# Kernel tuning notes

Hardware: AMD Instinct MI355X
Metric: run time of the kernel (lower is better)

The kernel has to match this reference:

```python
import jax, jax.numpy as jnp
import numpy as np

B, T, D, H, L = 64, 4096, 128, 128, 2


def setup_inputs() -> dict:
    key = jax.random.key(0)
    ks = jax.random.split(key, 9)
    s = 1.0 / np.sqrt(H)
    return {
        "x": jax.random.normal(ks[0], (B, T, D), dtype=jnp.float32),
        "W_ih0": jax.random.normal(ks[1], (3 * H, D), dtype=jnp.float32) * s,
        "W_hh0": jax.random.normal(ks[2], (3 * H, H), dtype=jnp.float32) * s,
        "b_ih0": jax.random.normal(ks[3], (3 * H,), dtype=jnp.float32) * s,
        "b_hh0": jax.random.normal(ks[4], (3 * H,), dtype=jnp.float32) * s,
        "W_ih1": jax.random.normal(ks[5], (3 * H, H), dtype=jnp.float32) * s,
        "W_hh1": jax.random.normal(ks[6], (3 * H, H), dtype=jnp.float32) * s,
        "b_ih1": jax.random.normal(ks[7], (3 * H,), dtype=jnp.float32) * s,
        "b_hh1": jax.random.normal(ks[8], (3 * H,), dtype=jnp.float32) * s,
    }


def _gru_cell(h, xt, W_ih, W_hh, b_ih, b_hh):
    # torch.nn.GRUCell math; gates packed as [r, z, n] along 3H.
    gi = xt @ W_ih.T + b_ih            # [B, 3H]
    gh = h @ W_hh.T + b_hh             # [B, 3H]
    i_r, i_z, i_n = jnp.split(gi, 3, axis=-1)
    h_r, h_z, h_n = jnp.split(gh, 3, axis=-1)
    r = jax.nn.sigmoid(i_r + h_r)
    z = jax.nn.sigmoid(i_z + h_z)
    n = jnp.tanh(i_n + r * h_n)
    return (1.0 - z) * n + z * h


def reference(x, W_ih0, W_hh0, b_ih0, b_hh0, W_ih1, W_hh1, b_ih1, b_hh1):
    h0 = jnp.zeros((L, x.shape[0], H), dtype=x.dtype)
    params = ((W_ih0, W_hh0, b_ih0, b_hh0), (W_ih1, W_hh1, b_ih1, b_hh1))

    def step(h, xt):
        # h: [L, B, H]; xt: [B, D]
        inp = xt
        new_h = []
        for l in range(L):
            hl = _gru_cell(h[l], inp, *params[l])
            new_h.append(hl)
            inp = hl
        return jnp.stack(new_h, axis=0), None

    xs = jnp.swapaxes(x, 0, 1)  # [T, B, D]
    h_final, _ = jax.lax.scan(step, h0, xs)
    return h_final  # [L, B, H]
```

## Files before the change

### kernel.cpp

```cpp
#include <hip/hip_runtime.h>
#include <cmath>


#define Bsz  64
#define Tlen 4096
#define Din  128
#define Hd   128

typedef __attribute__((ext_vector_type(8))) short short8;
typedef __attribute__((ext_vector_type(4))) short short4v;
typedef __attribute__((ext_vector_type(4))) float float4v;

#define MFMA16(a, b, c) __builtin_amdgcn_mfma_f32_16x16x32_bf16((a), (b), (c), 0, 0, 0)

static __device__ __forceinline__ short f2bf(float f) {
  unsigned u = __builtin_bit_cast(unsigned, f);
  u = (u + 0x7FFFu + ((u >> 16) & 1u)) >> 16;
  return (short)u;
}

static __device__ __forceinline__ float sigm(float x) {
  return __builtin_amdgcn_rcpf(1.0f + __expf(-x));
}

static __device__ __forceinline__ float tanh_f(float x) {
  x = fmaxf(x, -30.0f);
  float e = __expf(-2.0f * x);
  return (1.0f - e) * __builtin_amdgcn_rcpf(1.0f + e);
}

static __device__ __forceinline__ short8 loadw8(const float* __restrict__ p) {
  short8 r;
  #pragma unroll
  for (int j = 0; j < 8; ++j) r[j] = f2bf(p[j]);
  return r;
}

#define STRIDE 520

__global__ __launch_bounds__(512, 2) void gru_scan(
    const float* __restrict__ x,
    const float* __restrict__ Wih0, const float* __restrict__ Whh0,
    const float* __restrict__ bih0, const float* __restrict__ bhh0,
    const float* __restrict__ Wih1, const float* __restrict__ Whh1,
    const float* __restrict__ bih1, const float* __restrict__ bhh1,
    float* __restrict__ out) {
  __shared__ alignas(16) short Abuf[16 * STRIDE];

  const int tid   = threadIdx.x;
  const int wave  = tid >> 6;
  const int lane  = tid & 63;
  const int lc    = lane & 15;
  const int quad  = lane >> 4;
  const int q8    = quad * 8;
  const int bbase = blockIdx.x * 16;

  const int nr = wave * 16 + lc;
  const int nz = 128 + wave * 16 + lc;
  const int nn = 256 + wave * 16 + lc;

  short8 fr0[8], fz0[8], fin0[4], fhn0[4];
  short8 fr1[8], fz1[8], fin1[4], fhn1[4];
  #pragma unroll
  for (int s = 0; s < 4; ++s) {
    const int k = 32 * s + q8;
    fr0[s]     = loadw8(Wih0 + nr * Din + k);
    fz0[s]     = loadw8(Wih0 + nz * Din + k);
    fin0[s]    = loadw8(Wih0 + nn * Din + k);
    fr0[s + 4] = loadw8(Whh0 + nr * Hd + k);
    fz0[s + 4] = loadw8(Whh0 + nz * Hd + k);
    fhn0[s]    = loadw8(Whh0 + nn * Hd + k);
    fr1[s]     = loadw8(Wih1 + nr * Hd + k);
    fz1[s]     = loadw8(Wih1 + nz * Hd + k);
    fin1[s]    = loadw8(Wih1 + nn * Hd + k);
    fr1[s + 4] = loadw8(Whh1 + nr * Hd + k);
    fz1[s + 4] = loadw8(Whh1 + nz * Hd + k);
    fhn1[s]    = loadw8(Whh1 + nn * Hd + k);
  }

  const float br0 = bih0[nr] + bhh0[nr];
  const float bz0 = bih0[nz] + bhh0[nz];
  const float bi0 = bih0[nn];
  const float bh0 = bhh0[nn];
  const float br1 = bih1[nr] + bhh1[nr];
  const float bz1 = bih1[nz] + bhh1[nz];
  const float bi1 = bih1[nn];
  const float bh1 = bhh1[nn];

  for (int i = tid; i < 16 * STRIDE; i += 512) Abuf[i] = 0;
  __syncthreads();

  const int xrow = tid >> 5;
  const int xd   = (tid & 31) * 4;
  const float* xbase = x + (size_t)(bbase + xrow) * Tlen * Din + xd;
  {
    const float4v xv = *(const float4v*)xbase;
    short4v s4;
    #pragma unroll
    for (int j = 0; j < 4; ++j) s4[j] = f2bf(xv[j]);
    *(short4v*)&Abuf[xrow * STRIDE + xd] = s4;
  }
  __syncthreads();

  float h0p[4] = {0.f, 0.f, 0.f, 0.f};
  float h1p[4] = {0.f, 0.f, 0.f, 0.f};
  const int aoff = lc * STRIDE + q8;

  #pragma unroll 2
  for (int t = 0; t < Tlen; ++t) {
    const int tn = (t + 1 < Tlen) ? t + 1 : t;
    const float4v xv = *(const float4v*)(xbase + (size_t)tn * Din);

    float4v ar = {0.f, 0.f, 0.f, 0.f}, az = {0.f, 0.f, 0.f, 0.f};
    float4v ain = {0.f, 0.f, 0.f, 0.f}, ahn = {0.f, 0.f, 0.f, 0.f};
    #pragma unroll
    for (int s = 0; s < 4; ++s) {
      const short8 a = *(const short8*)&Abuf[aoff + 32 * s];
      ar  = MFMA16(a, fr0[s], ar);
      az  = MFMA16(a, fz0[s], az);
      ain = MFMA16(a, fin0[s], ain);
    }
    #pragma unroll
    for (int s = 0; s < 4; ++s) {
      const short8 a = *(const short8*)&Abuf[aoff + 128 + 32 * s];
      ar  = MFMA16(a, fr0[s + 4], ar);
      az  = MFMA16(a, fz0[s + 4], az);
      ahn = MFMA16(a, fhn0[s], ahn);
    }
    __syncthreads();

    float h0n[4];
    #pragma unroll
    for (int i = 0; i < 4; ++i) {
      const float r  = sigm(ar[i] + br0);
      const float z  = sigm(az[i] + bz0);
      const float nn_ = tanh_f(ain[i] + bi0 + r * (ahn[i] + bh0));
      h0n[i] = z * (h0p[i] - nn_) + nn_;
      h0p[i] = h0n[i];
    }
    #pragma unroll
    for (int i = 0; i < 4; ++i)
      Abuf[(quad * 4 + i) * STRIDE + 128 + wave * 16 + lc] = f2bf(h0n[i]);
    {
      short4v s4;
      #pragma unroll
      for (int j = 0; j < 4; ++j) s4[j] = f2bf(xv[j]);
      *(short4v*)&Abuf[xrow * STRIDE + xd] = s4;
    }
    __syncthreads();

    const int rb = 256 + 128 * (t & 1);
    const int wb = 256 + 128 * ((t & 1) ^ 1);
    float4v cr = {0.f, 0.f, 0.f, 0.f}, cz = {0.f, 0.f, 0.f, 0.f};
    float4v cin = {0.f, 0.f, 0.f, 0.f}, chn = {0.f, 0.f, 0.f, 0.f};
    #pragma unroll
    for (int s = 0; s < 4; ++s) {
      const short8 a = *(const short8*)&Abuf[aoff + 128 + 32 * s];
      cr  = MFMA16(a, fr1[s], cr);
      cz  = MFMA16(a, fz1[s], cz);
      cin = MFMA16(a, fin1[s], cin);
    }
    #pragma unroll
    for (int s = 0; s < 4; ++s) {
      const short8 a = *(const short8*)&Abuf[aoff + rb + 32 * s];
      cr  = MFMA16(a, fr1[s + 4], cr);
      cz  = MFMA16(a, fz1[s + 4], cz);
      chn = MFMA16(a, fhn1[s], chn);
    }
    #pragma unroll
    for (int i = 0; i < 4; ++i) {
      const float r  = sigm(cr[i] + br1);
      const float z  = sigm(cz[i] + bz1);
      const float nn_ = tanh_f(cin[i] + bi1 + r * (chn[i] + bh1));
      const float h  = z * (h1p[i] - nn_) + nn_;
      h1p[i] = h;
      Abuf[(quad * 4 + i) * STRIDE + wb + wave * 16 + lc] = f2bf(h);
    }
  }

  #pragma unroll
  for (int i = 0; i < 4; ++i) {
    const int b = bbase + quad * 4 + i;
    const int h = wave * 16 + lc;
    out[b * Hd + h]            = h0p[i];
    out[Bsz * Hd + b * Hd + h] = h1p[i];
  }
}

extern "C" void kernel_launch(void* const* d_in, const int* in_sizes, int n_in,
                              void* d_out, int out_size, void* d_ws, size_t ws_size,
                              hipStream_t stream) {
  (void)in_sizes; (void)n_in; (void)out_size; (void)d_ws; (void)ws_size;
  gru_scan<<<4, 512, 0, stream>>>(
      (const float*)d_in[0],
      (const float*)d_in[1], (const float*)d_in[2],
      (const float*)d_in[3], (const float*)d_in[4],
      (const float*)d_in[5], (const float*)d_in[6],
      (const float*)d_in[7], (const float*)d_in[8],
      (float*)d_out);
}
```

Baseline: 8.490 ms.

## Software-pipeline GRU layers across phases with swizzled LDS and exp2 gates

Restructures the per-timestep loop into two phases so that layer-1 gate math for step t-1 is interleaved with layer-0 MFMAs for step t, and layer-0 gate math overlaps layer-1 MFMAs. This hides transcendental latency behind matrix work while keeping two barriers per step. It also replaces the padded row-major LDS layout with a fragment-ordered layout so each lane reads one contiguous short8. Gate activations fold log2(e) scaling into exp2 and packed bf16 conversions. The added prologue and epilogue make the ping-pong indexing more complex and easier to get wrong.

Measured after the change: 13.14 ms. 1.55x slower.

```diff
diff --git a/kernel.cpp b/kernel.cpp
--- a/kernel.cpp
+++ b/kernel.cpp
@@ -1,5 +1,4 @@
 #include <hip/hip_runtime.h>
-#include <cmath>
 
 
 #define Bsz  64
@@ -10,25 +9,33 @@
 typedef __attribute__((ext_vector_type(8))) short short8;
 typedef __attribute__((ext_vector_type(4))) short short4v;
 typedef __attribute__((ext_vector_type(4))) float float4v;
+typedef __attribute__((ext_vector_type(2))) unsigned int uintx2;
 
 #define MFMA16(a, b, c) __builtin_amdgcn_mfma_f32_16x16x32_bf16((a), (b), (c), 0, 0, 0)
 
+static __device__ __forceinline__ float fast_exp2(float x) {
+#if __has_builtin(__builtin_amdgcn_exp2f)
+  return __builtin_amdgcn_exp2f(x);
+#else
+  return exp2f(x);
+#endif
+}
+static __device__ __forceinline__ float fast_rcp(float x) {
+  return __builtin_amdgcn_rcpf(x);
+}
 static __device__ __forceinline__ short f2bf(float f) {
   unsigned u = __builtin_bit_cast(unsigned, f);
   u = (u + 0x7FFFu + ((u >> 16) & 1u)) >> 16;
   return (short)u;
 }
-
-static __device__ __forceinline__ float sigm(float x) {
-  return __builtin_amdgcn_rcpf(1.0f + __expf(-x));
-}
-
-static __device__ __forceinline__ float tanh_f(float x) {
-  x = fmaxf(x, -30.0f);
-  float e = __expf(-2.0f * x);
-  return (1.0f - e) * __builtin_amdgcn_rcpf(1.0f + e);
-}
-
+static __device__ __forceinline__ unsigned pk2bf(float a, float b) {
+#if __has_builtin(__builtin_amdgcn_cvt_pk_bf16_f32)
+  auto v = __builtin_amdgcn_cvt_pk_bf16_f32(a, b);
+  return __builtin_bit_cast(unsigned, v);
+#else
+  return (unsigned)(unsigned short)f2bf(a) | ((unsigned)(unsigned short)f2bf(b) << 16);
+#endif
+}
 static __device__ __forceinline__ short8 loadw8(const float* __restrict__ p) {
   short8 r;
   #pragma unroll
@@ -36,7 +43,6 @@
   return r;
 }
 
-#define STRIDE 520
 
 __global__ __launch_bounds__(512, 2) void gru_scan(
     const float* __restrict__ x,
@@ -45,7 +51,7 @@
     const float* __restrict__ Wih1, const float* __restrict__ Whh1,
     const float* __restrict__ bih1, const float* __restrict__ bhh1,
     float* __restrict__ out) {
-  __shared__ alignas(16) short Abuf[16 * STRIDE];
+  __shared__ alignas(16) short Abuf[10240];
 
   const int tid   = threadIdx.x;
   const int wave  = tid >> 6;
@@ -53,6 +59,7 @@
   const int lc    = lane & 15;
   const int quad  = lane >> 4;
   const int q8    = quad * 8;
+  const int lane8 = lane * 8;
   const int bbase = blockIdx.x * 16;
 
   const int nr = wave * 16 + lc;
@@ -78,112 +85,178 @@
     fhn1[s]    = loadw8(Whh1 + nn * Hd + k);
   }
 
-  const float br0 = bih0[nr] + bhh0[nr];
-  const float bz0 = bih0[nz] + bhh0[nz];
-  const float bi0 = bih0[nn];
-  const float bh0 = bhh0[nn];
-  const float br1 = bih1[nr] + bhh1[nr];
-  const float bz1 = bih1[nz] + bhh1[nz];
-  const float bi1 = bih1[nn];
-  const float bh1 = bhh1[nn];
-
-  for (int i = tid; i < 16 * STRIDE; i += 512) Abuf[i] = 0;
-  __syncthreads();
-
-  const int xrow = tid >> 5;
-  const int xd   = (tid & 31) * 4;
-  const float* xbase = x + (size_t)(bbase + xrow) * Tlen * Din + xd;
+  const float nL  = -1.44269504088896f;
+  const float n2L = -2.88539008177793f;
+  const float kr0 = nL * (bih0[nr] + bhh0[nr]);
+  const float kz0 = nL * (bih0[nz] + bhh0[nz]);
+  const float ki0 = n2L * bih0[nn];
+  const float kh0 = n2L * bhh0[nn];
+  const float kr1 = nL * (bih1[nr] + bhh1[nr]);
+  const float kz1 = nL * (bih1[nz] + bhh1[nz]);
+  const float ki1 = n2L * bih1[nn];
+  const float kh1 = n2L * bhh1[nn];
+
+  const int col    = wave * 16 + lc;
+  const int hwbase = ((col >> 5) << 9) + (((col >> 3) & 3) << 7) + (col & 7);
+
+  const int xrow = (tid >> 1) & 15;
+  const int xcol = ((tid >> 7) << 5) + (((tid >> 5) & 3) << 3) + ((tid & 1) << 2);
+  const float* xg = x + (size_t)(bbase + xrow) * (Tlen * Din) + xcol;
+  const int xw = 4 * tid;
+
   {
-    const float4v xv = *(const float4v*)xbase;
-    short4v s4;
-    #pragma unroll
-    for (int j = 0; j < 4; ++j) s4[j] = f2bf(xv[j]);
-    *(short4v*)&Abuf[xrow * STRIDE + xd] = s4;
-  }
-  __syncthreads();
-
+    int* zb = (int*)Abuf;
+    #pragma unroll
+    for (int i = 0; i < 8; ++i) zb[1024 + tid + 512 * i] = 0;
+    const float4v v0 = *(const float4v*)(xg);
+    const unsigned p0 = pk2bf(v0[0], v0[1]);
+    const unsigned p1 = pk2bf(v0[2], v0[3]);
+    uintx2 pp = {p0, p1};
+    *(short4v*)&Abuf[xw] = __builtin_bit_cast(short4v, pp);
+  }
+  __syncthreads();
+
+  const float4v Z4 = {0.f, 0.f, 0.f, 0.f};
+  float4v Ar = Z4, Az = Z4, Ain = Z4, Ahn = Z4;
+  float4v Cr = Z4, Cz = Z4, Cin = Z4, Chn = Z4;
   float h0p[4] = {0.f, 0.f, 0.f, 0.f};
   float h1p[4] = {0.f, 0.f, 0.f, 0.f};
-  const int aoff = lc * STRIDE + q8;
-
-  #pragma unroll 2
-  for (int t = 0; t < Tlen; ++t) {
-    const int tn = (t + 1 < Tlen) ? t + 1 : t;
-    const float4v xv = *(const float4v*)(xbase + (size_t)tn * Din);
-
-    float4v ar = {0.f, 0.f, 0.f, 0.f}, az = {0.f, 0.f, 0.f, 0.f};
-    float4v ain = {0.f, 0.f, 0.f, 0.f}, ahn = {0.f, 0.f, 0.f, 0.f};
+  float4v xv;
+  int t;
+
+#define GATE(acc_r, acc_z, acc_in, acc_hn, KR, KZ, KI, KH, hp, dst, S)        \
+  {                                                                           \
+    const float er = fast_exp2(fmaf((acc_r)[S], nL, (KR)));                   \
+    const float rr = fast_rcp(1.0f + er);                                     \
+    const float ez = fast_exp2(fmaf((acc_z)[S], nL, (KZ)));                   \
+    const float zz = fast_rcp(1.0f + ez);                                     \
+    float vv = fmaf(rr, fmaf((acc_hn)[S], n2L, (KH)),                         \
+                    fmaf((acc_in)[S], n2L, (KI)));                            \
+    vv = fminf(vv, 126.0f);                                                   \
+    const float e2 = fast_exp2(vv);                                           \
+    const float nn_ = (1.0f - e2) * fast_rcp(1.0f + e2);                      \
+    (dst)[S] = fmaf(zz, (hp)[S] - nn_, nn_);                                  \
+    (hp)[S] = (dst)[S];                                                       \
+  }
+
+#define PH_A(P, DOV1)                                                         \
+  {                                                                           \
+    const int tn = (t + 1 < Tlen) ? (t + 1) : (Tlen - 1);                     \
+    xv = *(const float4v*)(xg + (size_t)tn * Din);                            \
+    Ar = Z4; Az = Z4; Ain = Z4; Ahn = Z4;                                     \
+    float h1n[4];                                                             \
+    _Pragma("unroll")                                                         \
+    for (int s = 0; s < 4; ++s) {                                             \
+      const short8 a = *(const short8*)&Abuf[s * 512 + lane8];                \
+      Ar  = MFMA16(a, fr0[s], Ar);                                            \
+      Az  = MFMA16(a, fz0[s], Az);                                            \
+      Ain = MFMA16(a, fin0[s], Ain);                                          \
+      if (DOV1) GATE(Cr, Cz, Cin, Chn, kr1, kz1, ki1, kh1, h1p, h1n, s)       \
+    }                                                                         \
+    _Pragma("unroll")                                                         \
+    for (int s = 0; s < 4; ++s) {                                             \
+      const short8 a =                                                        \
+          *(const short8*)&Abuf[2048 + ((P) ^ 1) * 2048 + s * 512 + lane8];   \
+      Ar  = MFMA16(a, fr0[4 + s], Ar);                                        \
+      Az  = MFMA16(a, fz0[4 + s], Az);                                        \
+      Ahn = MFMA16(a, fhn0[s], Ahn);                                          \
+      if ((DOV1) && (s & 1)) {                                                \
+        const unsigned pk = pk2bf(h1n[s - 1], h1n[s]);                        \
+        Abuf[6144 + (P) * 2048 + hwbase + (quad * 4 + s - 1) * 8] =           \
+            (short)pk;                                                        \
+        Abuf[6144 + (P) * 2048 + hwbase + (quad * 4 + s) * 8] =               \
+            (short)(pk >> 16);                                                \
+      }                                                                       \
+    }                                                                         \
+  }                                                                           \
+  __syncthreads();
+
+#define PH_B(P, DOC)                                                          \
+  {                                                                           \
+    float h0n[4];                                                             \
+    if (DOC) { Cr = Z4; Cz = Z4; Cin = Z4; Chn = Z4; }                        \
+    _Pragma("unroll")                                                         \
+    for (int s = 0; s < 4; ++s) {                                             \
+      if (DOC) {                                                              \
+        const short8 a =                                                      \
+            *(const short8*)&Abuf[2048 + ((P) ^ 1) * 2048 + s * 512 + lane8]; \
+        Cr  = MFMA16(a, fr1[s], Cr);                                          \
+        Cz  = MFMA16(a, fz1[s], Cz);                                          \
+        Cin = MFMA16(a, fin1[s], Cin);                                        \
+      }                                                                       \
+      GATE(Ar, Az, Ain, Ahn, kr0, kz0, ki0, kh0, h0p, h0n, s)                 \
+    }                                                                         \
+    _Pragma("unroll")                                                         \
+    for (int s = 0; s < 4; ++s) {                                             \
+      if (DOC) {                                                              \
+        const short8 a =                                                      \
+            *(const short8*)&Abuf[6144 + (P) * 2048 + s * 512 + lane8];       \
+        Cr  = MFMA16(a, fr1[4 + s], Cr);                                      \
+        Cz  = MFMA16(a, fz1[4 + s], Cz);                                      \
+        Chn = MFMA16(a, fhn1[s], Chn);                                        \
+      }                                                                       \
+      if (s & 1) {                                                            \
+        const unsigned pk = pk2bf(h0n[s - 1], h0n[s]);                        \
+        Abuf[2048 + (P) * 2048 + hwbase + (quad * 4 + s - 1) * 8] =           \
+            (short)pk;                                                        \
+        Abuf[2048 + (P) * 2048 + hwbase + (quad * 4 + s) * 8] =               \
+            (short)(pk >> 16);                                                \
+      }                                                                       \
+    }                                                                         \
+    {                                                                         \
+      const unsigned p0 = pk2bf(xv[0], xv[1]);                                \
+      const unsigned p1 = pk2bf(xv[2], xv[3]);                                \
+      uintx2 pp = {p0, p1};                                                   \
+      *(short4v*)&Abuf[xw] = __builtin_bit_cast(short4v, pp);                 \
+    }                                                                         \
+  }                                                                           \
+  __syncthreads();
+
+  t = 0; PH_A(0, 0) PH_B(0, 0)
+  t = 1; PH_A(1, 0) PH_B(1, 1)
+  for (int tt = 2; tt < Tlen; tt += 2) {
+    t = tt;     PH_A(0, 1) PH_B(0, 1)
+    t = tt + 1; PH_A(1, 1) PH_B(1, 1)
+  }
+
+  {
+    float h1n[4];
+    #pragma unroll
+    for (int s = 0; s < 4; ++s) GATE(Cr, Cz, Cin, Chn, kr1, kz1, ki1, kh1, h1p, h1n, s)
+    #pragma unroll
+    for (int s = 1; s < 4; s += 2) {
+      const unsigned pk = pk2bf(h1n[s - 1], h1n[s]);
+      Abuf[6144 + hwbase + (quad * 4 + s - 1) * 8] = (short)pk;
+      Abuf[6144 + hwbase + (quad * 4 + s) * 8]     = (short)(pk >> 16);
+    }
+  }
+  __syncthreads();
+  {
+    Cr = Z4; Cz = Z4; Cin = Z4; Chn = Z4;
     #pragma unroll
     for (int s = 0; s < 4; ++s) {
-      const short8 a = *(const short8*)&Abuf[aoff + 32 * s];
-      ar  = MFMA16(a, fr0[s], ar);
-      az  = MFMA16(a, fz0[s], az);
-      ain = MFMA16(a, fin0[s], ain);
+      const short8 a = *(const short8*)&Abuf[4096 + s * 512 + lane8];
+      Cr  = MFMA16(a, fr1[s], Cr);
+      Cz  = MFMA16(a, fz1[s], Cz);
+      Cin = MFMA16(a, fin1[s], Cin);
     }
     #pragma unroll
     for (int s = 0; s < 4; ++s) {
-      const short8 a = *(const short8*)&Abuf[aoff + 128 + 32 * s];
-      ar  = MFMA16(a, fr0[s + 4], ar);
-      az  = MFMA16(a, fz0[s + 4], az);
-      ahn = MFMA16(a, fhn0[s], ahn);
+      const short8 a = *(const short8*)&Abuf[6144 + s * 512 + lane8];
+      Cr  = MFMA16(a, fr1[4 + s], Cr);
+      Cz  = MFMA16(a, fz1[4 + s], Cz);
+      Chn = MFMA16(a, fhn1[s], Chn);
     }
-    __syncthreads();
-
-    float h0n[4];
-    #pragma unroll
-    for (int i = 0; i < 4; ++i) {
-      const float r  = sigm(ar[i] + br0);
-      const float z  = sigm(az[i] + bz0);
-      const float nn_ = tanh_f(ain[i] + bi0 + r * (ahn[i] + bh0));
-      h0n[i] = z * (h0p[i] - nn_) + nn_;
-      h0p[i] = h0n[i];
-    }
-    #pragma unroll
-    for (int i = 0; i < 4; ++i)
-      Abuf[(quad * 4 + i) * STRIDE + 128 + wave * 16 + lc] = f2bf(h0n[i]);
-    {
-      short4v s4;
-      #pragma unroll
-      for (int j = 0; j < 4; ++j) s4[j] = f2bf(xv[j]);
-      *(short4v*)&Abuf[xrow * STRIDE + xd] = s4;
-    }
-    __syncthreads();
-
-    const int rb = 256 + 128 * (t & 1);
-    const int wb = 256 + 128 * ((t & 1) ^ 1);
-    float4v cr = {0.f, 0.f, 0.f, 0.f}, cz = {0.f, 0.f, 0.f, 0.f};
-    float4v cin = {0.f, 0.f, 0.f, 0.f}, chn = {0.f, 0.f, 0.f, 0.f};
-    #pragma unroll
-    for (int s = 0; s < 4; ++s) {
-      const short8 a = *(const short8*)&Abuf[aoff + 128 + 32 * s];
-      cr  = MFMA16(a, fr1[s], cr);
-      cz  = MFMA16(a, fz1[s], cz);
-      cin = MFMA16(a, fin1[s], cin);
-    }
-    #pragma unroll
-    for (int s = 0; s < 4; ++s) {
-      const short8 a = *(const short8*)&Abuf[aoff + rb + 32 * s];
-      cr  = MFMA16(a, fr1[s + 4], cr);
-      cz  = MFMA16(a, fz1[s + 4], cz);
-      chn = MFMA16(a, fhn1[s], chn);
-    }
-    #pragma unroll
-    for (int i = 0; i < 4; ++i) {
-      const float r  = sigm(cr[i] + br1);
-      const float z  = sigm(cz[i] + bz1);
-      const float nn_ = tanh_f(cin[i] + bi1 + r * (chn[i] + bh1));
-      const float h  = z * (h1p[i] - nn_) + nn_;
-      h1p[i] = h;
-      Abuf[(quad * 4 + i) * STRIDE + wb + wave * 16 + lc] = f2bf(h);
-    }
+    float h1n[4];
+    #pragma unroll
+    for (int s = 0; s < 4; ++s) GATE(Cr, Cz, Cin, Chn, kr1, kz1, ki1, kh1, h1p, h1n, s)
   }
 
   #pragma unroll
   for (int i = 0; i < 4; ++i) {
     const int b = bbase + quad * 4 + i;
-    const int h = wave * 16 + lc;
-    out[b * Hd + h]            = h0p[i];
-    out[Bsz * Hd + b * Hd + h] = h1p[i];
+    out[b * Hd + col]            = h0p[i];
+    out[Bsz * Hd + b * Hd + col] = h1p[i];
   }
 }
 
```

## Split waves into per-layer groups and pipeline the two GRU layers across timesteps

Applied to the files above, without the earlier changes.

Waves 0-3 now compute layer 0 and waves 4-7 compute layer 1. Layer 1 runs one step behind layer 0, so each timestep does both layers concurrently with two barriers. Before, the layers ran in sequence with a dependent barrier between them. The input projection for the next step is issued after the hidden-state barrier so it overlaps the following step. Shared memory moves to a pre-swizzled, double-buffered layout that allows contiguous lane8 fragment loads, and the gate math uses exp2/rcp with biases pre-scaled by log2(e), plus packed bf16 conversion for x. Each wave now holds the weights for only one layer but covers twice the output columns, and the schedule adds two pipeline-fill iterations.

Measured after the change: 7.178 ms. 1.18x faster.

```diff
diff --git a/kernel.cpp b/kernel.cpp
--- a/kernel.cpp
+++ b/kernel.cpp
@@ -1,34 +1,40 @@
 #include <hip/hip_runtime.h>
-#include <cmath>
-
-
+
+
+#define Tlen 4096
+#define Hd   128
 #define Bsz  64
-#define Tlen 4096
-#define Din  128
-#define Hd   128
 
 typedef __attribute__((ext_vector_type(8))) short short8;
 typedef __attribute__((ext_vector_type(4))) short short4v;
 typedef __attribute__((ext_vector_type(4))) float float4v;
+typedef __attribute__((ext_vector_type(2))) unsigned int uint2v;
 
 #define MFMA16(a, b, c) __builtin_amdgcn_mfma_f32_16x16x32_bf16((a), (b), (c), 0, 0, 0)
 
+static __device__ __forceinline__ float fast_exp2(float x) {
+#if __has_builtin(__builtin_amdgcn_exp2f)
+  return __builtin_amdgcn_exp2f(x);
+#else
+  return exp2f(x);
+#endif
+}
+static __device__ __forceinline__ float fast_rcp(float x) {
+  return __builtin_amdgcn_rcpf(x);
+}
 static __device__ __forceinline__ short f2bf(float f) {
   unsigned u = __builtin_bit_cast(unsigned, f);
   u = (u + 0x7FFFu + ((u >> 16) & 1u)) >> 16;
   return (short)u;
 }
-
-static __device__ __forceinline__ float sigm(float x) {
-  return __builtin_amdgcn_rcpf(1.0f + __expf(-x));
-}
-
-static __device__ __forceinline__ float tanh_f(float x) {
-  x = fmaxf(x, -30.0f);
-  float e = __expf(-2.0f * x);
-  return (1.0f - e) * __builtin_amdgcn_rcpf(1.0f + e);
-}
-
+static __device__ __forceinline__ unsigned pk2bf(float a, float b) {
+#if __has_builtin(__builtin_amdgcn_cvt_pk_bf16_f32)
+  auto v = __builtin_amdgcn_cvt_pk_bf16_f32(a, b);
+  return __builtin_bit_cast(unsigned, v);
+#else
+  return (unsigned)(unsigned short)f2bf(a) | ((unsigned)(unsigned short)f2bf(b) << 16);
+#endif
+}
 static __device__ __forceinline__ short8 loadw8(const float* __restrict__ p) {
   short8 r;
   #pragma unroll
@@ -36,7 +42,10 @@
   return r;
 }
 
-#define STRIDE 520
+#define XB   0
+#define H0B  4096
+#define H1B  8192
+#define BLK  2048
 
 __global__ __launch_bounds__(512, 2) void gru_scan(
     const float* __restrict__ x,
@@ -45,7 +54,7 @@
     const float* __restrict__ Wih1, const float* __restrict__ Whh1,
     const float* __restrict__ bih1, const float* __restrict__ bhh1,
     float* __restrict__ out) {
-  __shared__ alignas(16) short Abuf[16 * STRIDE];
+  __shared__ alignas(16) short Abuf[12288];
 
   const int tid   = threadIdx.x;
   const int wave  = tid >> 6;
@@ -53,137 +62,155 @@
   const int lc    = lane & 15;
   const int quad  = lane >> 4;
   const int q8    = quad * 8;
+  const int lane8 = lane * 8;
   const int bbase = blockIdx.x * 16;
 
-  const int nr = wave * 16 + lc;
-  const int nz = 128 + wave * 16 + lc;
-  const int nn = 256 + wave * 16 + lc;
-
-  short8 fr0[8], fz0[8], fin0[4], fhn0[4];
-  short8 fr1[8], fz1[8], fin1[4], fhn1[4];
+  const int wgrp = wave >> 2;
+  const int w4   = wave & 3;
+
+  const float* Wi = wgrp ? Wih1 : Wih0;
+  const float* Wh = wgrp ? Whh1 : Whh0;
+  const float* bi = wgrp ? bih1 : bih0;
+  const float* bh = wgrp ? bhh1 : bhh0;
+
+  short8 fxr[2][4], fxz[2][4], fxn[2][4];
+  short8 fhr[2][4], fhz[2][4], fhn[2][4];
+  float kr[2], kz[2], ki[2], kh[2];
+  const float nL  = -1.44269504088896f;
+  const float n2L = -2.88539008177793f;
+  #pragma unroll
+  for (int G = 0; G < 2; ++G) {
+    const int c = 32 * w4 + 16 * G + lc;
+    #pragma unroll
+    for (int s = 0; s < 4; ++s) {
+      const int k = 32 * s + q8;
+      fxr[G][s] = loadw8(Wi + (c)       * Hd + k);
+      fxz[G][s] = loadw8(Wi + (128 + c) * Hd + k);
+      fxn[G][s] = loadw8(Wi + (256 + c) * Hd + k);
+      fhr[G][s] = loadw8(Wh + (c)       * Hd + k);
+      fhz[G][s] = loadw8(Wh + (128 + c) * Hd + k);
+      fhn[G][s] = loadw8(Wh + (256 + c) * Hd + k);
+    }
+    kr[G] = nL  * (bi[c] + bh[c]);
+    kz[G] = nL  * (bi[128 + c] + bh[128 + c]);
+    ki[G] = n2L * bi[256 + c];
+    kh[G] = n2L * bh[256 + c];
+  }
+
+  const int hsel = wgrp ? H1B : H0B;
+  const int isel = wgrp ? H0B : XB;
+
+  int hw[2];
+  #pragma unroll
+  for (int G = 0; G < 2; ++G)
+    hw[G] = w4 * 512 + (2 * G + (lc >> 3)) * 128 + (lc & 7);
+
+  const int xrow = tid >> 5;
+  const int xk0  = 4 * (tid & 31);
+  const int xwoff = (xk0 >> 5) * 512 + ((xk0 >> 3) & 3) * 128 + xrow * 8 + (xk0 & 7);
+  const float* xg = x + (size_t)(bbase + xrow) * (Tlen * Hd) + xk0;
+
+  const int glo = wgrp ? 2 : 0;
+  const int ghi = glo + Tlen;
+
+  {
+    int* zb = (int*)Abuf;
+    #pragma unroll
+    for (int i = 0; i < 8; ++i) zb[2048 + tid + 512 * i] = 0;
+    const float4v v0 = *(const float4v*)(xg);
+    const float4v v1 = *(const float4v*)(xg + Hd);
+    uint2v p0 = {pk2bf(v0[0], v0[1]), pk2bf(v0[2], v0[3])};
+    uint2v p1 = {pk2bf(v1[0], v1[1]), pk2bf(v1[2], v1[3])};
+    *(short4v*)&Abuf[XB + xwoff]       = __builtin_bit_cast(short4v, p0);
+    *(short4v*)&Abuf[XB + BLK + xwoff] = __builtin_bit_cast(short4v, p1);
+  }
+  __syncthreads();
+
+  const float4v Z4 = {0.f, 0.f, 0.f, 0.f};
+  float4v ar[2], az[2], an[2], ah[2];
+  float4v hp[2] = {Z4, Z4};
+
+  #pragma unroll
+  for (int G = 0; G < 2; ++G) { ar[G] = Z4; az[G] = Z4; an[G] = Z4; ah[G] = Z4; }
   #pragma unroll
   for (int s = 0; s < 4; ++s) {
-    const int k = 32 * s + q8;
-    fr0[s]     = loadw8(Wih0 + nr * Din + k);
-    fz0[s]     = loadw8(Wih0 + nz * Din + k);
-    fin0[s]    = loadw8(Wih0 + nn * Din + k);
-    fr0[s + 4] = loadw8(Whh0 + nr * Hd + k);
-    fz0[s + 4] = loadw8(Whh0 + nz * Hd + k);
-    fhn0[s]    = loadw8(Whh0 + nn * Hd + k);
-    fr1[s]     = loadw8(Wih1 + nr * Hd + k);
-    fz1[s]     = loadw8(Wih1 + nz * Hd + k);
-    fin1[s]    = loadw8(Wih1 + nn * Hd + k);
-    fr1[s + 4] = loadw8(Whh1 + nr * Hd + k);
-    fz1[s + 4] = loadw8(Whh1 + nz * Hd + k);
-    fhn1[s]    = loadw8(Whh1 + nn * Hd + k);
-  }
-
-  const float br0 = bih0[nr] + bhh0[nr];
-  const float bz0 = bih0[nz] + bhh0[nz];
-  const float bi0 = bih0[nn];
-  const float bh0 = bhh0[nn];
-  const float br1 = bih1[nr] + bhh1[nr];
-  const float bz1 = bih1[nz] + bhh1[nz];
-  const float bi1 = bih1[nn];
-  const float bh1 = bhh1[nn];
-
-  for (int i = tid; i < 16 * STRIDE; i += 512) Abuf[i] = 0;
-  __syncthreads();
-
-  const int xrow = tid >> 5;
-  const int xd   = (tid & 31) * 4;
-  const float* xbase = x + (size_t)(bbase + xrow) * Tlen * Din + xd;
-  {
-    const float4v xv = *(const float4v*)xbase;
-    short4v s4;
-    #pragma unroll
-    for (int j = 0; j < 4; ++j) s4[j] = f2bf(xv[j]);
-    *(short4v*)&Abuf[xrow * STRIDE + xd] = s4;
-  }
-  __syncthreads();
-
-  float h0p[4] = {0.f, 0.f, 0.f, 0.f};
-  float h1p[4] = {0.f, 0.f, 0.f, 0.f};
-  const int aoff = lc * STRIDE + q8;
-
-  #pragma unroll 2
-  for (int t = 0; t < Tlen; ++t) {
-    const int tn = (t + 1 < Tlen) ? t + 1 : t;
-    const float4v xv = *(const float4v*)(xbase + (size_t)tn * Din);
-
-    float4v ar = {0.f, 0.f, 0.f, 0.f}, az = {0.f, 0.f, 0.f, 0.f};
-    float4v ain = {0.f, 0.f, 0.f, 0.f}, ahn = {0.f, 0.f, 0.f, 0.f};
+    const short8 a = *(const short8*)&Abuf[isel + s * 512 + lane8];
+    #pragma unroll
+    for (int G = 0; G < 2; ++G) {
+      ar[G] = MFMA16(a, fxr[G][s], ar[G]);
+      az[G] = MFMA16(a, fxz[G][s], az[G]);
+      an[G] = MFMA16(a, fxn[G][s], an[G]);
+    }
+  }
+
+  for (int t = 0; t < Tlen + 2; ++t) {
+    const int par  = (t & 1) * BLK;
+    const int parx = BLK - par;
+
+    const int tn = (t + 2 < Tlen) ? (t + 2) : (Tlen - 1);
+    const float4v xv = *(const float4v*)(xg + (size_t)tn * Hd);
+    const int hrd = hsel + parx;
     #pragma unroll
     for (int s = 0; s < 4; ++s) {
-      const short8 a = *(const short8*)&Abuf[aoff + 32 * s];
-      ar  = MFMA16(a, fr0[s], ar);
-      az  = MFMA16(a, fz0[s], az);
-      ain = MFMA16(a, fin0[s], ain);
-    }
+      const short8 a = *(const short8*)&Abuf[hrd + s * 512 + lane8];
+      #pragma unroll
+      for (int G = 0; G < 2; ++G) {
+        ar[G] = MFMA16(a, fhr[G][s], ar[G]);
+        az[G] = MFMA16(a, fhz[G][s], az[G]);
+        ah[G] = MFMA16(a, fhn[G][s], ah[G]);
+      }
+    }
+    __syncthreads();
+
+    if (t >= glo && t < ghi) {
+      const int wr = hsel + par;
+      #pragma unroll
+      for (int G = 0; G < 2; ++G) {
+        #pragma unroll
+        for (int i = 0; i < 4; ++i) {
+          const float er = fast_exp2(fmaf(ar[G][i], nL, kr[G]));
+          const float rr = fast_rcp(1.0f + er);
+          const float ez = fast_exp2(fmaf(az[G][i], nL, kz[G]));
+          const float zz = fast_rcp(1.0f + ez);
+          float vv = fmaf(rr, fmaf(ah[G][i], n2L, kh[G]),
+                          fmaf(an[G][i], n2L, ki[G]));
+          vv = fminf(vv, 126.0f);
+          const float e2 = fast_exp2(vv);
+          const float nn = (1.0f - e2) * fast_rcp(1.0f + e2);
+          const float hn = fmaf(zz, hp[G][i] - nn, nn);
+          hp[G][i] = hn;
+          Abuf[wr + hw[G] + (quad * 4 + i) * 8] = f2bf(hn);
+        }
+      }
+    }
+    {
+      uint2v pp = {pk2bf(xv[0], xv[1]), pk2bf(xv[2], xv[3])};
+      *(short4v*)&Abuf[XB + par + xwoff] = __builtin_bit_cast(short4v, pp);
+    }
+    const int ird = isel + parx;
+    #pragma unroll
+    for (int G = 0; G < 2; ++G) { ar[G] = Z4; az[G] = Z4; an[G] = Z4; ah[G] = Z4; }
     #pragma unroll
     for (int s = 0; s < 4; ++s) {
-      const short8 a = *(const short8*)&Abuf[aoff + 128 + 32 * s];
-      ar  = MFMA16(a, fr0[s + 4], ar);
-      az  = MFMA16(a, fz0[s + 4], az);
-      ahn = MFMA16(a, fhn0[s], ahn);
+      const short8 a = *(const short8*)&Abuf[ird + s * 512 + lane8];
+      #pragma unroll
+      for (int G = 0; G < 2; ++G) {
+        ar[G] = MFMA16(a, fxr[G][s], ar[G]);
+        az[G] = MFMA16(a, fxz[G][s], az[G]);
+        an[G] = MFMA16(a, fxn[G][s], an[G]);
+      }
     }
     __syncthreads();
-
-    float h0n[4];
+  }
+
+  #pragma unroll
+  for (int G = 0; G < 2; ++G) {
+    const int u = 32 * w4 + 16 * G + lc;
     #pragma unroll
     for (int i = 0; i < 4; ++i) {
-      const float r  = sigm(ar[i] + br0);
-      const float z  = sigm(az[i] + bz0);
-      const float nn_ = tanh_f(ain[i] + bi0 + r * (ahn[i] + bh0));
-      h0n[i] = z * (h0p[i] - nn_) + nn_;
-      h0p[i] = h0n[i];
-    }
-    #pragma unroll
-    for (int i = 0; i < 4; ++i)
-      Abuf[(quad * 4 + i) * STRIDE + 128 + wave * 16 + lc] = f2bf(h0n[i]);
-    {
-      short4v s4;
-      #pragma unroll
-      for (int j = 0; j < 4; ++j) s4[j] = f2bf(xv[j]);
-      *(short4v*)&Abuf[xrow * STRIDE + xd] = s4;
-    }
-    __syncthreads();
-
-    const int rb = 256 + 128 * (t & 1);
-    const int wb = 256 + 128 * ((t & 1) ^ 1);
-    float4v cr = {0.f, 0.f, 0.f, 0.f}, cz = {0.f, 0.f, 0.f, 0.f};
-    float4v cin = {0.f, 0.f, 0.f, 0.f}, chn = {0.f, 0.f, 0.f, 0.f};
-    #pragma unroll
-    for (int s = 0; s < 4; ++s) {
-      const short8 a = *(const short8*)&Abuf[aoff + 128 + 32 * s];
-      cr  = MFMA16(a, fr1[s], cr);
-      cz  = MFMA16(a, fz1[s], cz);
-      cin = MFMA16(a, fin1[s], cin);
-    }
-    #pragma unroll
-    for (int s = 0; s < 4; ++s) {
-      const short8 a = *(const short8*)&Abuf[aoff + rb + 32 * s];
-      cr  = MFMA16(a, fr1[s + 4], cr);
-      cz  = MFMA16(a, fz1[s + 4], cz);
-      chn = MFMA16(a, fhn1[s], chn);
-    }
-    #pragma unroll
-    for (int i = 0; i < 4; ++i) {
-      const float r  = sigm(cr[i] + br1);
-      const float z  = sigm(cz[i] + bz1);
-      const float nn_ = tanh_f(cin[i] + bi1 + r * (chn[i] + bh1));
-      const float h  = z * (h1p[i] - nn_) + nn_;
-      h1p[i] = h;
-      Abuf[(quad * 4 + i) * STRIDE + wb + wave * 16 + lc] = f2bf(h);
-    }
-  }
-
-  #pragma unroll
-  for (int i = 0; i < 4; ++i) {
-    const int b = bbase + quad * 4 + i;
-    const int h = wave * 16 + lc;
-    out[b * Hd + h]            = h0p[i];
-    out[Bsz * Hd + b * Hd + h] = h1p[i];
+      const int b = bbase + quad * 4 + i;
+      out[wgrp * (Bsz * Hd) + b * Hd + u] = hp[G][i];
+    }
   }
 }
 
```
